# Performance work log

Measured on AMD Instinct MI355X. Metric: run time of the kernel, lower is better.

The kernel has to match this reference:

```python
import jax, jax.numpy as jnp
import numpy as np

NUM_HEADS = 16
THETA = 10000.0


def _rope(x, pos):
    # x: (B, H, S, d_k), pos: (B, S) int
    d_k = x.shape[-1]
    freqs = 1.0 / (THETA ** (jnp.arange(0, d_k, 2, dtype=jnp.float32) / d_k))  # (d_k/2,)
    angles = pos[..., None].astype(jnp.float32) * freqs  # (B, S, d_k/2)
    cos = jnp.cos(angles)[:, None, :, :]  # (B, 1, S, d_k/2) broadcast over heads
    sin = jnp.sin(angles)[:, None, :, :]
    x1 = x[..., 0::2]
    x2 = x[..., 1::2]
    out1 = x1 * cos - x2 * sin
    out2 = x1 * sin + x2 * cos
    # interleave back: (..., d_k/2, 2) -> (..., d_k)
    return jnp.stack((out1, out2), axis=-1).reshape(x.shape)


def setup_inputs() -> dict:
    key = jax.random.key(0)
    ks = jax.random.split(key, 6)
    B, S, D = 4, 2048, 1024
    x = jax.random.normal(ks[0], (B, S, D), dtype=jnp.float32)
    token_positions = jnp.sort(jax.random.randint(ks[1], (B, S), 0, S), axis=-1).astype(jnp.int32)
    Wq = jax.random.normal(ks[2], (D, D), dtype=jnp.float32) * (D ** -0.5)
    Wk = jax.random.normal(ks[3], (D, D), dtype=jnp.float32) * (D ** -0.5)
    Wv = jax.random.normal(ks[4], (D, D), dtype=jnp.float32) * (D ** -0.5)
    Wo = jax.random.normal(ks[5], (D, D), dtype=jnp.float32) * (D ** -0.5)
    return {"x": x, "token_positions": token_positions, "Wq": Wq, "Wk": Wk, "Wv": Wv, "Wo": Wo}


def reference(x, token_positions, Wq, Wk, Wv, Wo):
    B, S, D = x.shape
    H = NUM_HEADS
    d_k = D // H
    # projections: y = x @ W.T  (Linear stores weight as (d_out, d_in))
    q = jnp.einsum('bsd,od->bso', x, Wq).reshape(B, S, H, d_k).transpose(0, 2, 1, 3)
    k = jnp.einsum('bsd,od->bso', x, Wk).reshape(B, S, H, d_k).transpose(0, 2, 1, 3)
    v = jnp.einsum('bsd,od->bso', x, Wv).reshape(B, S, H, d_k).transpose(0, 2, 1, 3)
    q = _rope(q, token_positions)
    k = _rope(k, token_positions)
    scores = jnp.einsum('bhqd,bhkd->bhqk', q, k) / jnp.sqrt(jnp.float32(d_k))
    causal = jnp.tril(jnp.ones((S, S), dtype=bool))
    scores = jnp.where(causal, scores, -jnp.inf)
    attn = jax.nn.softmax(scores, axis=-1)
    attn = jnp.nan_to_num(attn, nan=0.0)
    out = jnp.einsum('bhqk,bhkd->bhqd', attn, v)
    out = out.transpose(0, 2, 1, 3).reshape(B, S, D)
    return jnp.einsum('bso,do->bsd', out, Wo)
```

## Files before the change

### kernel.cpp

```cpp
#include <hip/hip_runtime.h>
#include <stdint.h>

#define SEQ 2048
#define NH  16
#define DK  64
#define DM  1024
#define C2SM 0.18033688011112042f

typedef __bf16 bf16x8 __attribute__((ext_vector_type(8)));
typedef float  f32x4  __attribute__((ext_vector_type(4)));
typedef float  f32x16 __attribute__((ext_vector_type(16)));
typedef int    iv2    __attribute__((ext_vector_type(2)));
typedef void __attribute__((address_space(3))) lds_void;
typedef const void __attribute__((address_space(1))) glb_void;

__device__ __forceinline__ unsigned short f2b(float f) {
  unsigned int u = __float_as_uint(f);
  u += 0x7fffu + ((u >> 16) & 1u);
  return (unsigned short)(u >> 16);
}
__device__ __forceinline__ float b2f(unsigned short h) {
  return __uint_as_float(((unsigned int)h) << 16);
}
__device__ __forceinline__ void gload_lds16(const void* g, void* lds) {
  __builtin_amdgcn_global_load_lds((glb_void*)(uintptr_t)g,
                                   (lds_void*)(unsigned int)(uintptr_t)lds,
                                   16, 0, 0);
}
__device__ __forceinline__ unsigned int cvtpk(float lo, float hi) {
  unsigned int r;
  asm("v_cvt_pk_bf16_f32 %0, %1, %2" : "=v"(r) : "v"(lo), "v"(hi));
  return r;
}
__device__ __forceinline__ iv2 pl32swap(int a, int b) {
  return __builtin_amdgcn_permlane32_swap(a, b, false, false);
}

__global__ __launch_bounds__(256) void k_cvt(const float* __restrict__ src,
                                             unsigned short* __restrict__ dst, int n4) {
  int i = blockIdx.x * 256 + threadIdx.x;
  if (i >= n4) return;
  float4 v = ((const float4*)src)[i];
  uint2 o;
  o.x = (unsigned int)f2b(v.x) | ((unsigned int)f2b(v.y) << 16);
  o.y = (unsigned int)f2b(v.z) | ((unsigned int)f2b(v.w) << 16);
  ((uint2*)dst)[i] = o;
}

__global__ __launch_bounds__(256) void k_cvtw(const float* __restrict__ w0,
                                              const float* __restrict__ w1,
                                              const float* __restrict__ w2,
                                              const float* __restrict__ w3,
                                              unsigned short* __restrict__ dst) {
  int i = blockIdx.x * 256 + threadIdx.x;
  const float* s = (i < 524288) ? ((i < 262144) ? w0 : w1)
                                : ((i < 786432) ? w2 : w3);
  float4 v = ((const float4*)s)[i & 262143];
  uint2 o;
  o.x = (unsigned int)f2b(v.x) | ((unsigned int)f2b(v.y) << 16);
  o.y = (unsigned int)f2b(v.z) | ((unsigned int)f2b(v.w) << 16);
  ((uint2*)dst)[i] = o;
}

__global__ __launch_bounds__(256) void k_tab(float2* __restrict__ tab) {
  int i = blockIdx.x * 256 + threadIdx.x;
  int p = i >> 5, f = i & 31;
  float freq = powf(10000.0f, -(float)(2 * f) / (float)DK);
  float ang = (float)p * freq;
  tab[i] = make_float2(cosf(ang), sinf(ang));
}

template <int MODE>
__global__ __launch_bounds__(256) void k_gemm(const unsigned short* __restrict__ A,
                                              const unsigned short* __restrict__ B,
                                              void* __restrict__ C, void* __restrict__ C2,
                                              const int* __restrict__ pos,
                                              const float2* __restrict__ tab,
                                              int M, int N, int K) {
  __shared__ __align__(16) unsigned short As[3][4096];
  __shared__ __align__(16) unsigned short Bs[3][4096];
  const int tid = threadIdx.x;
  const int wid = tid >> 6, lane = tid & 63;
  const int lr = lane & 15, lk = lane >> 4;
  const int wr = wid >> 1, wc = wid & 1;
  const int m0 = blockIdx.x * 128, n0 = blockIdx.y * 128;
  const int r0 = tid >> 2;
  const int csw = (((tid & 3) ^ ((r0 >> 1) & 3)) << 3);
  const int ss = ((lk ^ ((lr >> 1) & 3)) << 3);
  f32x4 acc[4][4] = {};

#define GSTAGE(bi, k0)                                                       \
  do {                                                                       \
    gload_lds16(A + (size_t)(m0 + r0) * K + (k0) + csw, &As[bi][wid * 512]); \
    gload_lds16(A + (size_t)(m0 + 64 + r0) * K + (k0) + csw,                 \
                &As[bi][2048 + wid * 512]);                                  \
    gload_lds16(B + (size_t)(n0 + r0) * K + (k0) + csw, &Bs[bi][wid * 512]); \
    gload_lds16(B + (size_t)(n0 + 64 + r0) * K + (k0) + csw,                 \
                &Bs[bi][2048 + wid * 512]);                                  \
  } while (0)

  const int nt = K >> 5;
  GSTAGE(0, 0);
  if (nt > 1) {
    GSTAGE(1, 32);
    asm volatile("s_waitcnt vmcnt(4)" ::: "memory");
  } else {
    asm volatile("s_waitcnt vmcnt(0)" ::: "memory");
  }
  __builtin_amdgcn_s_barrier();
  int c0 = 0, c1 = 1, c2 = 2;
  for (int t = 0; t < nt; ++t) {
    if (t + 2 < nt) GSTAGE(c2, (t + 2) * 32);
    bf16x8 af[4], bfv[4];
#pragma unroll
    for (int i = 0; i < 4; ++i)
      af[i] = *(const bf16x8*)&As[c0][(wr * 64 + i * 16 + lr) * 32 + ss];
#pragma unroll
    for (int j = 0; j < 4; ++j)
      bfv[j] = *(const bf16x8*)&Bs[c0][(wc * 64 + j * 16 + lr) * 32 + ss];
    __builtin_amdgcn_s_setprio(1);
#pragma unroll
    for (int i = 0; i < 4; ++i)
#pragma unroll
      for (int j = 0; j < 4; ++j)
        acc[i][j] = __builtin_amdgcn_mfma_f32_16x16x32_bf16(af[i], bfv[j], acc[i][j], 0, 0, 0);
    __builtin_amdgcn_s_setprio(0);
    if (t + 1 < nt) {
      if (t + 2 < nt)
        asm volatile("s_waitcnt vmcnt(4)" ::: "memory");
      else
        asm volatile("s_waitcnt vmcnt(0)" ::: "memory");
      __builtin_amdgcn_s_barrier();
    }
    int tmp = c0; c0 = c1; c1 = c2; c2 = tmp;
  }
#undef GSTAGE

  if (MODE == 1) {
#pragma unroll
    for (int i = 0; i < 4; ++i) {
      const int rbase = m0 + wr * 64 + i * 16 + lk * 4;
#pragma unroll
      for (int j = 0; j < 4; ++j) {
        const int col = n0 + wc * 64 + j * 16 + lr;
#pragma unroll
        for (int r = 0; r < 4; ++r)
          ((float*)C)[(size_t)(rbase + r) * N + col] = acc[i][j][r];
      }
    }
  } else {
    const int tt = n0 >> 10;
    if (tt == 2) {
#pragma unroll
      for (int i = 0; i < 4; ++i) {
        const int rbase = m0 + wr * 64 + i * 16 + lk * 4;
        const int bb = rbase >> 11;
#pragma unroll
        for (int j = 0; j < 4; ++j) {
          const int col = n0 + wc * 64 + j * 16 + lr;
          const int h = (col >> 6) & 15, d = col & 63;
#pragma unroll
          for (int r = 0; r < 4; ++r) {
            const int s = (rbase + r) & (SEQ - 1);
            ((unsigned short*)C2)[((((size_t)bb * NH + h) * SEQ) + s) * DK + d] =
                f2b(acc[i][j][r]);
          }
        }
      }
    } else {
#pragma unroll
      for (int i = 0; i < 4; ++i) {
        const int rbase = m0 + wr * 64 + i * 16 + lk * 4;
        const int bb = rbase >> 11;
        int prr[4];
#pragma unroll
        for (int r = 0; r < 4; ++r)
          prr[r] = pos[bb * SEQ + ((rbase + r) & (SEQ - 1))];
#pragma unroll
        for (int j = 0; j < 4; ++j) {
          const int col = n0 + wc * 64 + j * 16 + lr;
          const int h = (col >> 6) & 15, d = col & 63;
          const int f = d >> 1;
#pragma unroll
          for (int r = 0; r < 4; ++r) {
            float v = acc[i][j][r];
            float pv = __shfl_xor(v, 1);
            float2 cs = tab[(size_t)prr[r] * 32 + f];
            float o = (d & 1) ? __builtin_fmaf(pv, cs.y, v * cs.x)
                              : __builtin_fmaf(-pv, cs.y, v * cs.x);
            const int s = (rbase + r) & (SEQ - 1);
            ((unsigned short*)C)[(size_t)tt * 8388608 +
                                 ((((size_t)bb * NH + h) * SEQ) + s) * DK + d] = f2b(o);
          }
        }
      }
    }
  }
}

__global__ __launch_bounds__(256) void k_vt(const unsigned short* __restrict__ V,
                                            unsigned short* __restrict__ VT) {
  __shared__ __align__(16) unsigned short T[64 * 64];
  const int bh = blockIdx.y, st = blockIdx.x;
  const unsigned short* Vp = V + (size_t)bh * SEQ * DK + (size_t)st * 64 * DK;
  unsigned short* Tp = VT + (size_t)bh * DK * SEQ + st * 64;
#pragma unroll
  for (int it = 0; it < 2; ++it) {
    int c = it * 256 + threadIdx.x;
    int s = c >> 3, slot = c & 7;
    uint4 v = *(const uint4*)&Vp[s * DK + slot * 8];
    *(uint4*)&T[s * 64 + ((slot ^ (s & 7)) << 3)] = v;
  }
  __syncthreads();
#pragma unroll
  for (int it = 0; it < 2; ++it) {
    int c = it * 256 + threadIdx.x;
    int d = c >> 3, sq = (c & 7) << 3;
    unsigned int w[4];
#pragma unroll
    for (int k = 0; k < 4; ++k) {
      int r0 = sq + 2 * k, r1 = sq + 2 * k + 1;
      unsigned int lo = T[r0 * 64 + ((((d >> 3) ^ (r0 & 7)) << 3) | (d & 7))];
      unsigned int hi = T[r1 * 64 + ((((d >> 3) ^ (r1 & 7)) << 3) | (d & 7))];
      w[k] = lo | (hi << 16);
    }
    *(uint4*)&Tp[(size_t)d * SEQ + sq] = make_uint4(w[0], w[1], w[2], w[3]);
  }
}

__global__ __launch_bounds__(128) void k_attn(const unsigned short* __restrict__ Q,
                                              const unsigned short* __restrict__ K,
                                              const unsigned short* __restrict__ VT,
                                              unsigned short* __restrict__ O) {
  __shared__ __align__(16) unsigned short Ks[2][64 * 64];
  __shared__ __align__(16) unsigned short Vs[2][64 * 64];
  const int tid = threadIdx.x, wid = tid >> 6, lane = tid & 63;
  const int l31 = lane & 31, hi = lane >> 5;
  const int n = blockIdx.x;
  const int bh = n & 63, x = n >> 6;
  const unsigned short* Qp = Q + (size_t)bh * SEQ * DK;
  const unsigned short* Kp = K + (size_t)bh * SEQ * DK;
  const unsigned short* Vp = VT + (size_t)bh * DK * SEQ;
  const int b = bh >> 4, h = bh & (NH - 1);

#define STAGE(bi, kb)                                                          \
  do {                                                                         \
    _Pragma("unroll") for (int i = 0; i < 4; ++i) {                            \
      const int c = i * 128 + tid;                                             \
      const int row = c >> 3, sl = ((c & 7) ^ (row & 7)) << 3;                 \
      gload_lds16(Kp + (size_t)((kb) + row) * DK + sl,                         \
                  &Ks[bi][(i * 128 + wid * 64) * 8]);                          \
      gload_lds16(Vp + (size_t)row * SEQ + (kb) + sl,                          \
                  &Vs[bi][(i * 128 + wid * 64) * 8]);                          \
    }                                                                          \
  } while (0)

#pragma unroll
  for (int pass = 0; pass < 2; ++pass) {
    const int qt = pass ? 31 - x : x;
    const int qw = qt * 64 + wid * 32;
    const int qrow = qw + l31;
    bf16x8 qf[4];
#pragma unroll
    for (int ks = 0; ks < 4; ++ks)
      qf[ks] = *(const bf16x8*)&Qp[(size_t)qrow * DK + ks * 16 + hi * 8];
    f32x16 oacc[2] = {};
    float m_ = -1e30f, l_ = 0.f;
    const int ntiles = qt + 1;
    STAGE(0, 0);
    for (int kt = 0; kt < ntiles; ++kt) {
      const int cur = kt & 1;
      const int kb = kt * 64;
      if (kt + 1 < ntiles) {
        STAGE(cur ^ 1, kb + 64);
        asm volatile("s_waitcnt vmcnt(8)" ::: "memory");
      } else {
        asm volatile("s_waitcnt vmcnt(0)" ::: "memory");
      }
      __builtin_amdgcn_s_barrier();
      {
        f32x16 sa[2];
        __builtin_amdgcn_s_setprio(1);
#pragma unroll
        for (int kg = 0; kg < 2; ++kg) {
          const int krow = kg * 32 + l31;
          f32x16 z = {};
#pragma unroll
          for (int ks = 0; ks < 4; ++ks) {
            bf16x8 kf = *(const bf16x8*)((const char*)&Ks[cur][0] + krow * 128 +
                                         (((2 * ks + hi) ^ (krow & 7)) << 4));
            z = __builtin_amdgcn_mfma_f32_32x32x16_bf16(kf, qf[ks], z, 0, 0, 0);
          }
          sa[kg] = z;
        }
        __builtin_amdgcn_s_setprio(0);
        if (kb + 64 > qw) {
          const int th0 = qrow - kb - 4 * hi;
#pragma unroll
          for (int kg = 0; kg < 2; ++kg) {
            const int th = th0 - kg * 32;
#pragma unroll
            for (int r = 0; r < 16; ++r) {
              const int cst = (r & 3) + 8 * (r >> 2);
              if (cst > th) sa[kg][r] = -1e30f;
            }
          }
        }
        float mx;
        {
          float a0 = fmaxf(fmaxf(sa[0][0], sa[0][1]), fmaxf(sa[0][2], sa[0][3]));
          float a1 = fmaxf(fmaxf(sa[0][4], sa[0][5]), fmaxf(sa[0][6], sa[0][7]));
          float a2 = fmaxf(fmaxf(sa[0][8], sa[0][9]), fmaxf(sa[0][10], sa[0][11]));
          float a3 = fmaxf(fmaxf(sa[0][12], sa[0][13]), fmaxf(sa[0][14], sa[0][15]));
          float a4 = fmaxf(fmaxf(sa[1][0], sa[1][1]), fmaxf(sa[1][2], sa[1][3]));
          float a5 = fmaxf(fmaxf(sa[1][4], sa[1][5]), fmaxf(sa[1][6], sa[1][7]));
          float a6 = fmaxf(fmaxf(sa[1][8], sa[1][9]), fmaxf(sa[1][10], sa[1][11]));
          float a7 = fmaxf(fmaxf(sa[1][12], sa[1][13]), fmaxf(sa[1][14], sa[1][15]));
          mx = fmaxf(fmaxf(fmaxf(a0, a1), fmaxf(a2, a3)),
                     fmaxf(fmaxf(a4, a5), fmaxf(a6, a7)));
          iv2 t = pl32swap(__float_as_int(mx), __float_as_int(mx));
          mx = fmaxf(__int_as_float(t.x), __int_as_float(t.y));
        }
        if (!__all(mx <= m_ + 16.f)) {
          const float mn = fmaxf(m_, mx);
          const float sc = __builtin_amdgcn_exp2f((m_ - mn) * C2SM);
          m_ = mn;
          l_ *= sc;
#pragma unroll
          for (int vg = 0; vg < 2; ++vg)
#pragma unroll
            for (int r = 0; r < 16; ++r) oacc[vg][r] *= sc;
        }
        const float mc = m_ * C2SM;
        float sum = 0.f;
#pragma unroll
        for (int kg = 0; kg < 2; ++kg)
#pragma unroll
          for (int r = 0; r < 16; ++r) {
            const float p = __builtin_amdgcn_exp2f(__builtin_fmaf(sa[kg][r], C2SM, -mc));
            sa[kg][r] = p;
            sum += p;
          }
        {
          iv2 t = pl32swap(__float_as_int(sum), __float_as_int(sum));
          l_ += __int_as_float(t.x) + __int_as_float(t.y);
        }
        __builtin_amdgcn_s_setprio(1);
#pragma unroll
        for (int kg = 0; kg < 2; ++kg)
#pragma unroll
          for (int ks2 = 0; ks2 < 2; ++ks2) {
            const int rb = ks2 * 8;
            unsigned wA = cvtpk(sa[kg][rb + 0], sa[kg][rb + 1]);
            unsigned wB = cvtpk(sa[kg][rb + 4], sa[kg][rb + 5]);
            unsigned wC = cvtpk(sa[kg][rb + 2], sa[kg][rb + 3]);
            unsigned wD = cvtpk(sa[kg][rb + 6], sa[kg][rb + 7]);
            iv2 r0 = pl32swap((int)wA, (int)wB);
            iv2 r1 = pl32swap((int)wC, (int)wD);
            union { uint4 u; bf16x8 v; } pu;
            pu.u = make_uint4((unsigned)r0.x, (unsigned)r1.x, (unsigned)r0.y, (unsigned)r1.y);
            const int ks = kg * 2 + ks2;
#pragma unroll
            for (int vg = 0; vg < 2; ++vg) {
              const int vrow = vg * 32 + l31;
              bf16x8 vf = *(const bf16x8*)((const char*)&Vs[cur][0] + vrow * 128 +
                                           (((2 * ks + hi) ^ (vrow & 7)) << 4));
              oacc[vg] = __builtin_amdgcn_mfma_f32_32x32x16_bf16(vf, pu.v, oacc[vg], 0, 0, 0);
            }
          }
        __builtin_amdgcn_s_setprio(0);
      }
      __builtin_amdgcn_s_barrier();
    }
    const float inv = 1.0f / l_;
    unsigned short* Orow = O + ((size_t)(b * SEQ + qrow)) * DM + h * DK;
#pragma unroll
    for (int vg = 0; vg < 2; ++vg)
#pragma unroll
      for (int j = 0; j < 4; ++j) {
        unsigned lo = cvtpk(oacc[vg][4 * j + 0] * inv, oacc[vg][4 * j + 1] * inv);
        unsigned hh = cvtpk(oacc[vg][4 * j + 2] * inv, oacc[vg][4 * j + 3] * inv);
        *(uint2*)&Orow[vg * 32 + 8 * j + 4 * hi] = make_uint2(lo, hh);
      }
  }
#undef STAGE
}

extern "C" void kernel_launch(void* const* d_in, const int* in_sizes, int n_in,
                              void* d_out, int out_size, void* d_ws, size_t ws_size,
                              hipStream_t stream) {
  const float* x = (const float*)d_in[0];
  const int* tp = (const int*)d_in[1];
  const float* W[4] = {(const float*)d_in[2], (const float*)d_in[3],
                       (const float*)d_in[4], (const float*)d_in[5]};
  unsigned short* xb = (unsigned short*)d_ws;
  unsigned short* wb0 = xb + (size_t)8192 * 1024;
  unsigned short* wb3 = wb0 + (size_t)3 * 1024 * 1024;
  float2* tab = (float2*)(wb0 + (size_t)4 * 1024 * 1024);
  unsigned short* Qb = (unsigned short*)(tab + SEQ * 32);
  unsigned short* Kb = Qb + (size_t)8192 * 1024;
  unsigned short* VTb = Kb + (size_t)8192 * 1024;
  unsigned short* Ob = VTb + (size_t)8192 * 1024;
  unsigned short* Vb = Ob;

  k_cvt<<<8192, 256, 0, stream>>>(x, xb, 2097152);
  k_cvtw<<<4096, 256, 0, stream>>>(W[0], W[1], W[2], W[3], wb0);
  k_tab<<<256, 256, 0, stream>>>(tab);
  k_gemm<3><<<dim3(64, 24), 256, 0, stream>>>(xb, wb0, Qb, Vb, tp, tab, 8192, 3072, 1024);
  k_vt<<<dim3(32, 64), 256, 0, stream>>>(Vb, VTb);
  k_attn<<<1024, 128, 0, stream>>>(Qb, Kb, VTb, Ob);
  k_gemm<1><<<dim3(64, 8), 256, 0, stream>>>(Ob, wb3, d_out, nullptr, nullptr, nullptr,
                                             8192, 1024, 1024);
}
```

Measured before the change: 181.0 us.

## Write V transposed from QKV GEMM and triple-buffer attention K/V loads

The QKV projection epilogue now writes V directly in transposed (d-major) layout with packed 4-element stores. This removes the separate k_vt transpose kernel and its extra global round trip. The attention kernel moves from double to triple buffering of K/V tiles in LDS, issuing loads two tiles ahead and waiting after compute. This gives loads more time to overlap MFMA work, at the cost of more LDS per block (48KB) and possibly lower occupancy. The transposed stores are strided by SEQ, so the GEMM epilogue writes for V are less coalesced.

```diff
diff --git a/kernel.cpp b/kernel.cpp
--- a/kernel.cpp
+++ b/kernel.cpp
@@ -155,16 +155,15 @@
       for (int i = 0; i < 4; ++i) {
         const int rbase = m0 + wr * 64 + i * 16 + lk * 4;
         const int bb = rbase >> 11;
+        const int s0 = rbase & (SEQ - 1);
 #pragma unroll
         for (int j = 0; j < 4; ++j) {
           const int col = n0 + wc * 64 + j * 16 + lr;
           const int h = (col >> 6) & 15, d = col & 63;
-#pragma unroll
-          for (int r = 0; r < 4; ++r) {
-            const int s = (rbase + r) & (SEQ - 1);
-            ((unsigned short*)C2)[((((size_t)bb * NH + h) * SEQ) + s) * DK + d] =
-                f2b(acc[i][j][r]);
-          }
+          uint2 pv;
+          pv.x = cvtpk(acc[i][j][0], acc[i][j][1]);
+          pv.y = cvtpk(acc[i][j][2], acc[i][j][3]);
+          *(uint2*)&((unsigned short*)C2)[(((size_t)bb * NH + h) * DK + d) * SEQ + s0] = pv;
         }
       }
     } else {
@@ -198,42 +197,12 @@
   }
 }
 
-__global__ __launch_bounds__(256) void k_vt(const unsigned short* __restrict__ V,
-                                            unsigned short* __restrict__ VT) {
-  __shared__ __align__(16) unsigned short T[64 * 64];
-  const int bh = blockIdx.y, st = blockIdx.x;
-  const unsigned short* Vp = V + (size_t)bh * SEQ * DK + (size_t)st * 64 * DK;
-  unsigned short* Tp = VT + (size_t)bh * DK * SEQ + st * 64;
-#pragma unroll
-  for (int it = 0; it < 2; ++it) {
-    int c = it * 256 + threadIdx.x;
-    int s = c >> 3, slot = c & 7;
-    uint4 v = *(const uint4*)&Vp[s * DK + slot * 8];
-    *(uint4*)&T[s * 64 + ((slot ^ (s & 7)) << 3)] = v;
-  }
-  __syncthreads();
-#pragma unroll
-  for (int it = 0; it < 2; ++it) {
-    int c = it * 256 + threadIdx.x;
-    int d = c >> 3, sq = (c & 7) << 3;
-    unsigned int w[4];
-#pragma unroll
-    for (int k = 0; k < 4; ++k) {
-      int r0 = sq + 2 * k, r1 = sq + 2 * k + 1;
-      unsigned int lo = T[r0 * 64 + ((((d >> 3) ^ (r0 & 7)) << 3) | (d & 7))];
-      unsigned int hi = T[r1 * 64 + ((((d >> 3) ^ (r1 & 7)) << 3) | (d & 7))];
-      w[k] = lo | (hi << 16);
-    }
-    *(uint4*)&Tp[(size_t)d * SEQ + sq] = make_uint4(w[0], w[1], w[2], w[3]);
-  }
-}
-
 __global__ __launch_bounds__(128) void k_attn(const unsigned short* __restrict__ Q,
                                               const unsigned short* __restrict__ K,
                                               const unsigned short* __restrict__ VT,
                                               unsigned short* __restrict__ O) {
-  __shared__ __align__(16) unsigned short Ks[2][64 * 64];
-  __shared__ __align__(16) unsigned short Vs[2][64 * 64];
+  __shared__ __align__(16) unsigned short Ks[3][64 * 64];
+  __shared__ __align__(16) unsigned short Vs[3][64 * 64];
   const int tid = threadIdx.x, wid = tid >> 6, lane = tid & 63;
   const int l31 = lane & 31, hi = lane >> 5;
   const int n = blockIdx.x;
@@ -267,17 +236,18 @@
     f32x16 oacc[2] = {};
     float m_ = -1e30f, l_ = 0.f;
     const int ntiles = qt + 1;
+    int c0 = 0, c1 = 1, c2 = 2;
     STAGE(0, 0);
+    if (ntiles > 1) {
+      STAGE(1, 64);
+      asm volatile("s_waitcnt vmcnt(8)" ::: "memory");
+    } else {
+      asm volatile("s_waitcnt vmcnt(0)" ::: "memory");
+    }
+    __builtin_amdgcn_s_barrier();
     for (int kt = 0; kt < ntiles; ++kt) {
-      const int cur = kt & 1;
       const int kb = kt * 64;
-      if (kt + 1 < ntiles) {
-        STAGE(cur ^ 1, kb + 64);
-        asm volatile("s_waitcnt vmcnt(8)" ::: "memory");
-      } else {
-        asm volatile("s_waitcnt vmcnt(0)" ::: "memory");
-      }
-      __builtin_amdgcn_s_barrier();
+      if (kt + 2 < ntiles) STAGE(c2, kb + 128);
       {
         f32x16 sa[2];
         __builtin_amdgcn_s_setprio(1);
@@ -287,7 +257,7 @@
           f32x16 z = {};
 #pragma unroll
           for (int ks = 0; ks < 4; ++ks) {
-            bf16x8 kf = *(const bf16x8*)((const char*)&Ks[cur][0] + krow * 128 +
+            bf16x8 kf = *(const bf16x8*)((const char*)&Ks[c0][0] + krow * 128 +
                                          (((2 * ks + hi) ^ (krow & 7)) << 4));
             z = __builtin_amdgcn_mfma_f32_32x32x16_bf16(kf, qf[ks], z, 0, 0, 0);
           }
@@ -363,14 +333,19 @@
 #pragma unroll
             for (int vg = 0; vg < 2; ++vg) {
               const int vrow = vg * 32 + l31;
-              bf16x8 vf = *(const bf16x8*)((const char*)&Vs[cur][0] + vrow * 128 +
+              bf16x8 vf = *(const bf16x8*)((const char*)&Vs[c0][0] + vrow * 128 +
                                            (((2 * ks + hi) ^ (vrow & 7)) << 4));
               oacc[vg] = __builtin_amdgcn_mfma_f32_32x32x16_bf16(vf, pu.v, oacc[vg], 0, 0, 0);
             }
           }
         __builtin_amdgcn_s_setprio(0);
       }
+      if (kt + 2 < ntiles)
+        asm volatile("s_waitcnt vmcnt(8)" ::: "memory");
+      else
+        asm volatile("s_waitcnt vmcnt(0)" ::: "memory");
       __builtin_amdgcn_s_barrier();
+      int tmp = c0; c0 = c1; c1 = c2; c2 = tmp;
     }
     const float inv = 1.0f / l_;
     unsigned short* Orow = O + ((size_t)(b * SEQ + qrow)) * DM + h * DK;
@@ -401,13 +376,11 @@
   unsigned short* Kb = Qb + (size_t)8192 * 1024;
   unsigned short* VTb = Kb + (size_t)8192 * 1024;
   unsigned short* Ob = VTb + (size_t)8192 * 1024;
-  unsigned short* Vb = Ob;
 
   k_cvt<<<8192, 256, 0, stream>>>(x, xb, 2097152);
   k_cvtw<<<4096, 256, 0, stream>>>(W[0], W[1], W[2], W[3], wb0);
   k_tab<<<256, 256, 0, stream>>>(tab);
-  k_gemm<3><<<dim3(64, 24), 256, 0, stream>>>(xb, wb0, Qb, Vb, tp, tab, 8192, 3072, 1024);
-  k_vt<<<dim3(32, 64), 256, 0, stream>>>(Vb, VTb);
+  k_gemm<3><<<dim3(64, 24), 256, 0, stream>>>(xb, wb0, Qb, VTb, tp, tab, 8192, 3072, 1024);
   k_attn<<<1024, 128, 0, stream>>>(Qb, Kb, VTb, Ob);
   k_gemm<1><<<dim3(64, 8), 256, 0, stream>>>(Ob, wb3, d_out, nullptr, nullptr, nullptr,
                                              8192, 1024, 1024);
```

Result: slower. 211.7 us (+17.0%).
